# Optimization experiments

Hardware: AMD Instinct MI355X
Metric: run time of the kernel (lower is better)

## Reference

```python
import jax, jax.numpy as jnp
import numpy as np

N, D, C = 8192, 256, 100
MARGIN = 1.0


def setup_inputs() -> dict:
    key = jax.random.key(0)
    k1, k2 = jax.random.split(key)
    features = jax.random.normal(k1, (N, D), dtype=jnp.float32)
    labels = jax.random.randint(k2, (N,), 0, C, dtype=jnp.int64)
    return {"features": features, "labels": labels}


def _pairwise_dist(f):
    # f: [N, D] L2-normalized rows. Euclidean distance matrix [N, N].
    sq = jnp.sum(f * f, axis=1)  # [N]
    d2 = sq[:, None] + sq[None, :] - 2.0 * (f @ f.T)
    d2 = jnp.maximum(d2, 0.0)
    # safe sqrt: zero distance (incl. diagonal) -> 0 with finite grad
    pos = d2 > 0.0
    return jnp.where(pos, jnp.sqrt(jnp.where(pos, d2, 1.0)), 0.0)


def reference(features, labels):
    # F.normalize(p=2, dim=1)
    norm = jnp.linalg.norm(features, axis=1, keepdims=True)
    f = features / jnp.maximum(norm, 1e-12)

    dist = _pairwise_dist(f)  # [N, N]

    onehot = jax.nn.one_hot(labels, C, dtype=f.dtype)  # [N, C]
    counts = jnp.sum(onehot, axis=0)  # [C]
    # S[a, b] = sum_{i in a, j in b} dist[i, j]
    S = onehot.T @ dist @ onehot  # [C, C]

    # intra: per-class mean over off-diagonal pairs (diag of dist is 0),
    # only classes with count > 1, then mean over those classes
    intra_valid = counts > 1.0
    intra_denom = jnp.where(intra_valid, counts * (counts - 1.0), 1.0)
    intra_per_class = jnp.diag(S) / intra_denom
    n_intra = jnp.sum(intra_valid.astype(f.dtype))
    intra = jnp.where(
        n_intra > 0,
        jnp.sum(jnp.where(intra_valid, intra_per_class, 0.0)) / jnp.maximum(n_intra, 1.0),
        0.0,
    )

    # inter: per class-pair (a < b, both present) mean distance, then mean over pairs
    pair_cnt = counts[:, None] * counts[None, :]
    inter_mat = S / jnp.where(pair_cnt > 0.0, pair_cnt, 1.0)
    present = counts > 0.0
    upper = jnp.triu(jnp.ones((C, C), dtype=bool), k=1)
    pair_mask = upper & present[:, None] & present[None, :]
    n_pairs = jnp.sum(pair_mask.astype(f.dtype))
    inter = jnp.where(
        n_pairs > 0,
        jnp.sum(jnp.where(pair_mask, inter_mat, 0.0)) / jnp.maximum(n_pairs, 1.0),
        1.0,
    )

    loss = jax.nn.relu(intra - inter + MARGIN)
    return loss  # scalar; .mean() of a scalar is itself
```

## Files before the change

### kernel.cpp

```cpp
#include <hip/hip_runtime.h>
#include <math.h>

#define N_ROWS 8192
#define D_DIM  256
#define C_CLS  100
#define BM 128
#define NSTRIP (N_ROWS / BM)
#define NBLK (NSTRIP * (NSTRIP + 1) / 2)
#define UPK (C_CLS * (C_CLS + 1) / 2)
#define MAXSEG 4

typedef __attribute__((ext_vector_type(4))) float floatx4;

__device__ __forceinline__ void gl2lds16(const void* g, void* l) {
    __builtin_amdgcn_global_load_lds(
        (const __attribute__((address_space(1))) void*)g,
        (__attribute__((address_space(3))) void*)l, 16, 0, 0);
}

__global__ void sort_k(const int* __restrict__ labels, int* __restrict__ dest,
                       int* __restrict__ slab, int* __restrict__ offs,
                       float* __restrict__ Ug, int* __restrict__ ctr) {
    __shared__ int h[C_CLS];
    __shared__ int incl[128];
    __shared__ int oS[C_CLS + 1];
    __shared__ int cur[C_CLS];
    const int t = threadIdx.x;
    if (t < C_CLS) h[t] = 0;
    __syncthreads();
    int myl[8];
#pragma unroll
    for (int u = 0; u < 8; ++u) myl[u] = labels[t + u * 1024];
#pragma unroll
    for (int u = 0; u < 8; ++u) atomicAdd(&h[myl[u]], 1);
    __syncthreads();
    if (t < 128) {
        const int lane = t & 63;
        int v = (t < C_CLS) ? h[t] : 0;
#pragma unroll
        for (int o = 1; o < 64; o <<= 1) {
            const int n = __shfl_up(v, o, 64);
            if (lane >= o) v += n;
        }
        incl[t] = v;
    }
    __syncthreads();
    if (t <= C_CLS)
        oS[t] = (t == 0) ? 0 : incl[t - 1] + ((t - 1) >= 64 ? incl[63] : 0);
    __syncthreads();
    if (t < C_CLS) cur[t] = oS[t];
    __syncthreads();
#pragma unroll
    for (int u = 0; u < 8; ++u) {
        const int i = t + u * 1024;
        const int pos = atomicAdd(&cur[myl[u]], 1);
        dest[i] = pos;
        slab[pos] = myl[u];
    }
    if (t < C_CLS + 1) offs[t] = oS[t];
    for (int e = t; e < UPK; e += 1024) Ug[e] = 0.f;
    if (t == 0) *ctr = 0;
}

__global__ void normalize_k(const float* __restrict__ in, const int* __restrict__ dest,
                            unsigned int* __restrict__ fnb8) {
    const int row  = blockIdx.x * 4 + (threadIdx.x >> 6);
    const int lane = threadIdx.x & 63;
    float4 v = ((const float4*)in)[row * 64 + lane];
    float s = v.x * v.x + v.y * v.y + v.z * v.z + v.w * v.w;
#pragma unroll
    for (int o = 32; o > 0; o >>= 1) s += __shfl_xor(s, o, 64);
    const float inv = 1.f / fmaxf(sqrtf(s), 1e-12f);
    const int d = dest[row];
    int pk = __builtin_amdgcn_cvt_pk_fp8_f32(v.x * inv, v.y * inv, 0, 0);
    pk     = __builtin_amdgcn_cvt_pk_fp8_f32(v.z * inv, v.w * inv, pk, 1);
    fnb8[d * 64 + lane] = (unsigned int)pk;
}

__global__ __launch_bounds__(256, 2)
void main_k(const unsigned char* __restrict__ fnb8, const int* __restrict__ slab,
            const int* __restrict__ offs_g, float* __restrict__ Ug,
            int* __restrict__ ctr, float* __restrict__ out) {
    __shared__ __align__(16) unsigned char smem[65536];
    unsigned char* const As = smem;
    unsigned char* const Bs = smem + 32768;
    float* const red   = (float*)smem;
    int*   const meta  = (int*)(smem + 4352);
    int*   const flag  = (int*)(smem + 4416);
    float* const rf    = (float*)(smem + 4432);
    int*   const ri    = (int*)(smem + 5456);
    int*   const soffs = (int*)(smem + 6480);

    const int t = threadIdx.x;

    int b = blockIdx.x, ti = 0, len = NSTRIP;
    while (b >= len) { b -= len; ++ti; --len; }
    const int tj = ti + b;
    const int i0 = ti * BM, j0 = tj * BM;

    const int lane = t & 63;
    const int w    = t >> 6;
    const int m0 = (w & 1) * 64, n0 = (w >> 1) * 64;
    const int lr = lane & 15, lq = lane >> 4;
    const int swz = (lr >> 1) & 7;

    int abase[4], bbase[4];
#pragma unroll
    for (int mb = 0; mb < 4; ++mb) abase[mb] = (m0 + mb * 16 + lr) * D_DIM;
#pragma unroll
    for (int nb = 0; nb < 4; ++nb) bbase[nb] = (n0 + nb * 16 + lr) * D_DIM;

#pragma unroll
    for (int u = 0; u < 8; ++u) {
        const int s = t + 256 * u;
        const int row = s >> 4;
        const int kc  = (s & 15) ^ ((row >> 1) & 7);
        gl2lds16(&fnb8[(size_t)(i0 + row) * D_DIM + kc * 16], &As[s * 16]);
    }
#pragma unroll
    for (int u = 0; u < 8; ++u) {
        const int s = t + 256 * u;
        const int row = s >> 4;
        const int kc  = (s & 15) ^ ((row >> 1) & 7);
        gl2lds16(&fnb8[(size_t)(j0 + row) * D_DIM + kc * 16], &Bs[s * 16]);
    }

    floatx4 acc[4][4];
#pragma unroll
    for (int mb = 0; mb < 4; ++mb)
#pragma unroll
        for (int nb = 0; nb < 4; ++nb) acc[mb][nb] = 0.f;

    __syncthreads();

#pragma unroll
    for (int si = 0; si < 8; ++si) {
        const int coff = ((((si * 2) + (lq >> 1)) ^ swz) << 4) + ((lq & 1) << 3);
        long a[4], bb[4];
#pragma unroll
        for (int mb = 0; mb < 4; ++mb) a[mb]  = *(const long*)&As[abase[mb] + coff];
#pragma unroll
        for (int nb = 0; nb < 4; ++nb) bb[nb] = *(const long*)&Bs[bbase[nb] + coff];
#pragma unroll
        for (int mb = 0; mb < 4; ++mb)
#pragma unroll
            for (int nb = 0; nb < 4; ++nb)
                acc[mb][nb] = __builtin_amdgcn_mfma_f32_16x16x32_fp8_fp8(
                    a[mb], bb[nb], acc[mb][nb], 0, 0, 0);
    }

    __syncthreads();

    if (t < C_CLS + 1) soffs[t] = offs_g[t];

    const bool diag = (ti == tj);
#pragma unroll
    for (int mb = 0; mb < 4; ++mb)
#pragma unroll
        for (int nb = 0; nb < 4; ++nb)
#pragma unroll
            for (int r = 0; r < 4; ++r) {
                const float g = acc[mb][nb][r];
                float dv = __builtin_amdgcn_sqrtf(fmaxf(2.f - 2.f * g, 0.f));
                const int rt = m0 + mb * 16 + lq * 4 + r;
                const int ct = n0 + nb * 16 + lr;
                if (diag && rt == ct) dv = 0.f;
                acc[mb][nb][r] = dv;
            }

    const int cA0 = __builtin_amdgcn_readfirstlane(slab[i0 + m0]);
    const int cA1 = __builtin_amdgcn_readfirstlane(slab[i0 + m0 + 63]);
    const int cB0 = __builtin_amdgcn_readfirstlane(slab[j0 + n0]);
    const int cB1 = __builtin_amdgcn_readfirstlane(slab[j0 + n0 + 63]);
    const int segsA = cA1 - cA0 + 1, segsB = cB1 - cB0 + 1;
    if (lane == 0) {
        meta[w * 4 + 0] = cA0; meta[w * 4 + 1] = cB0;
        meta[w * 4 + 2] = segsA; meta[w * 4 + 3] = segsB;
    }
    const float wscale = diag ? 1.f : 2.f;

    float rem[4][4];
#pragma unroll
    for (int mb = 0; mb < 4; ++mb)
#pragma unroll
        for (int r = 0; r < 4; ++r)
            rem[mb][r] = acc[mb][0][r] + acc[mb][1][r] + acc[mb][2][r] + acc[mb][3][r];

    __syncthreads();

    for (int sb = 0; sb < segsB; ++sb) {
        const int cb = cB0 + sb;
        float colsum[4][4];
        if (sb == segsB - 1) {
#pragma unroll
            for (int mb = 0; mb < 4; ++mb)
#pragma unroll
                for (int r = 0; r < 4; ++r) colsum[mb][r] = rem[mb][r];
        } else {
            const int rb0 = max(soffs[cb]     - j0, n0);
            const int rb1 = min(soffs[cb + 1] - j0, n0 + 64);
#pragma unroll
            for (int mb = 0; mb < 4; ++mb)
#pragma unroll
                for (int r = 0; r < 4; ++r) colsum[mb][r] = 0.f;
#pragma unroll
            for (int nb = 0; nb < 4; ++nb) {
                const int ct = n0 + nb * 16 + lr;
                const float mk = ((ct >= rb0) & (ct < rb1)) ? 1.f : 0.f;
#pragma unroll
                for (int mb = 0; mb < 4; ++mb)
#pragma unroll
                    for (int r = 0; r < 4; ++r)
                        colsum[mb][r] = fmaf(mk, acc[mb][nb][r], colsum[mb][r]);
            }
#pragma unroll
            for (int mb = 0; mb < 4; ++mb)
#pragma unroll
                for (int r = 0; r < 4; ++r) rem[mb][r] -= colsum[mb][r];
        }
        for (int sa = 0; sa < segsA; ++sa) {
            const int ca = cA0 + sa;
            const int ra0 = max(soffs[ca]     - i0, m0);
            const int ra1 = min(soffs[ca + 1] - i0, m0 + 64);
            float v = 0.f;
#pragma unroll
            for (int mb = 0; mb < 4; ++mb) {
                const int rtb = m0 + mb * 16 + lq * 4;
#pragma unroll
                for (int r = 0; r < 4; ++r) {
                    const int rt = rtb + r;
                    const bool ir = (rt >= ra0) & (rt < ra1);
                    v += ir ? colsum[mb][r] : 0.f;
                }
            }
            if (sa < MAXSEG && sb < MAXSEG) {
                v += __shfl_xor(v, 1, 64);
                v += __shfl_xor(v, 2, 64);
                if ((lane & 3) == 0)
                    red[(w * 16 + sb * MAXSEG + sa) * 17 + (lane >> 2)] = v;
            } else {
#pragma unroll
                for (int o = 32; o > 0; o >>= 1) v += __shfl_xor(v, o, 64);
                if (lane == 0 && v != 0.f) {
                    const int mn = min(ca, cb), mx = max(ca, cb);
                    atomicAdd(&Ug[mx + ((mn * (2 * C_CLS - 1 - mn)) >> 1)], wscale * v);
                }
            }
        }
    }

    __syncthreads();
    {
        const int combo = t >> 2, q = t & 3;
        const int wv = combo >> 4, sl = combo & 15;
        const float* rp = &red[(wv * 16 + sl) * 17];
        float s = rp[q * 4 + 0] + rp[q * 4 + 1] + rp[q * 4 + 2] + rp[q * 4 + 3];
        s += __shfl_xor(s, 1, 64);
        s += __shfl_xor(s, 2, 64);
        const int sa = sl & (MAXSEG - 1), sb = sl >> 2;
        if (q == 0 && sa < meta[wv * 4 + 2] && sb < meta[wv * 4 + 3] && s != 0.f) {
            const int ca = meta[wv * 4 + 0] + sa, cb = meta[wv * 4 + 1] + sb;
            const int mn = min(ca, cb), mx = max(ca, cb);
            atomicAdd(&Ug[mx + ((mn * (2 * C_CLS - 1 - mn)) >> 1)], wscale * s);
        }
    }

    __syncthreads();
    if (t == 0) {
        asm volatile("s_waitcnt vmcnt(0)" ::: "memory");
        *flag = (atomicAdd(ctr, 1) == NBLK - 1) ? 1 : 0;
    }
    __syncthreads();
    if (*flag) {
        __threadfence();
        float s_intra = 0.f; int n_intra = 0;
        if (t < C_CLS) {
            const int c = soffs[t + 1] - soffs[t];
            if (c > 1) {
                const int idx = t + ((t * (2 * C_CLS - 1 - t)) >> 1);
                s_intra = Ug[idx] / ((float)c * (float)(c - 1));
                n_intra = 1;
            }
        }
        float s_inter = 0.f; int n_pairs = 0;
        for (int p = t; p < C_CLS * C_CLS; p += 256) {
            const int a = p / C_CLS, b2 = p - a * C_CLS;
            if (b2 > a) {
                const int ca = soffs[a + 1] - soffs[a];
                const int cb = soffs[b2 + 1] - soffs[b2];
                if (ca > 0 && cb > 0) {
                    const int idx = b2 + ((a * (2 * C_CLS - 1 - a)) >> 1);
                    s_inter += 0.5f * Ug[idx] / ((float)ca * (float)cb);
                    ++n_pairs;
                }
            }
        }
        rf[t] = s_intra; ri[t] = n_intra; __syncthreads();
        for (int s2 = 128; s2 > 0; s2 >>= 1) {
            if (t < s2) { rf[t] += rf[t + s2]; ri[t] += ri[t + s2]; }
            __syncthreads();
        }
        const float intra_sum = rf[0]; const int intra_n = ri[0];
        __syncthreads();
        rf[t] = s_inter; ri[t] = n_pairs; __syncthreads();
        for (int s2 = 128; s2 > 0; s2 >>= 1) {
            if (t < s2) { rf[t] += rf[t + s2]; ri[t] += ri[t + s2]; }
            __syncthreads();
        }
        if (t == 0) {
            const float inter_sum = rf[0]; const int pairs_n = ri[0];
            const float intra = (intra_n > 0) ? intra_sum / (float)intra_n : 0.f;
            const float inter = (pairs_n > 0) ? inter_sum / (float)pairs_n : 1.f;
            out[0] = fmaxf(intra - inter + 1.0f, 0.f);
        }
    }
}

extern "C" void kernel_launch(void* const* d_in, const int* in_sizes, int n_in,
                              void* d_out, int out_size, void* d_ws, size_t ws_size,
                              hipStream_t stream) {
    const float* feats  = (const float*)d_in[0];
    const int*   labels = (const int*)d_in[1];
    float* out = (float*)d_out;

    char* p = (char*)d_ws;
    unsigned char* fnb8 = (unsigned char*)p;  p += (size_t)N_ROWS * D_DIM;
    int*   slab = (int*)p;  p += (size_t)N_ROWS * sizeof(int);
    int*   dest = (int*)p;  p += (size_t)N_ROWS * sizeof(int);
    int*   offs = (int*)p;  p += 128 * sizeof(int);
    float* Ug   = (float*)p;  p += ((UPK + 31) / 32) * 32 * sizeof(float);
    int*   ctr  = (int*)p;

    sort_k     <<<1, 1024, 0, stream>>>(labels, dest, slab, offs, Ug, ctr);
    normalize_k<<<N_ROWS / 4, 256, 0, stream>>>(feats, dest, (unsigned int*)fnb8);
    main_k     <<<NBLK, 256, 0, stream>>>(fnb8, slab, offs, Ug, ctr, out);
}
```

Before: 124.4 us.

## Fuse sort and normalize into one prep kernel, gather rows via permutation, split K

Merges the label counting-sort and the row normalization into a single launch. Normalized rows are now stored in original order, and the main kernel reads them through a permutation index, so normalization no longer waits on the sort. The main GEMM tile now loads K in two 128-wide chunks, which halves LDS use per block and allows 4 blocks per CU instead of 2. The costs are an indirect row gather, an extra barrier pair per K step, and a one-block sort that runs concurrently with the normalize blocks.

Result: faster. 117.7 us (-5.4%).

```diff
diff --git a/kernel.cpp b/kernel.cpp
--- a/kernel.cpp
+++ b/kernel.cpp
@@ -5,6 +5,7 @@
 #define D_DIM  256
 #define C_CLS  100
 #define BM 128
+#define BK 128
 #define NSTRIP (N_ROWS / BM)
 #define NBLK (NSTRIP * (NSTRIP + 1) / 2)
 #define UPK (C_CLS * (C_CLS + 1) / 2)
@@ -18,78 +19,76 @@
         (__attribute__((address_space(3))) void*)l, 16, 0, 0);
 }
 
-__global__ void sort_k(const int* __restrict__ labels, int* __restrict__ dest,
-                       int* __restrict__ slab, int* __restrict__ offs,
-                       float* __restrict__ Ug, int* __restrict__ ctr) {
-    __shared__ int h[C_CLS];
-    __shared__ int incl[128];
-    __shared__ int oS[C_CLS + 1];
-    __shared__ int cur[C_CLS];
-    const int t = threadIdx.x;
-    if (t < C_CLS) h[t] = 0;
-    __syncthreads();
-    int myl[8];
-#pragma unroll
-    for (int u = 0; u < 8; ++u) myl[u] = labels[t + u * 1024];
-#pragma unroll
-    for (int u = 0; u < 8; ++u) atomicAdd(&h[myl[u]], 1);
-    __syncthreads();
-    if (t < 128) {
-        const int lane = t & 63;
-        int v = (t < C_CLS) ? h[t] : 0;
-#pragma unroll
-        for (int o = 1; o < 64; o <<= 1) {
-            const int n = __shfl_up(v, o, 64);
-            if (lane >= o) v += n;
-        }
-        incl[t] = v;
-    }
-    __syncthreads();
-    if (t <= C_CLS)
-        oS[t] = (t == 0) ? 0 : incl[t - 1] + ((t - 1) >= 64 ? incl[63] : 0);
-    __syncthreads();
-    if (t < C_CLS) cur[t] = oS[t];
-    __syncthreads();
-#pragma unroll
-    for (int u = 0; u < 8; ++u) {
-        const int i = t + u * 1024;
-        const int pos = atomicAdd(&cur[myl[u]], 1);
-        dest[i] = pos;
-        slab[pos] = myl[u];
-    }
-    if (t < C_CLS + 1) offs[t] = oS[t];
-    for (int e = t; e < UPK; e += 1024) Ug[e] = 0.f;
-    if (t == 0) *ctr = 0;
+__global__ __launch_bounds__(256)
+void prep_k(const float* __restrict__ in, const int* __restrict__ labels,
+            unsigned int* __restrict__ fnb8, int* __restrict__ slab,
+            int* __restrict__ offs, int* __restrict__ perm,
+            float* __restrict__ Ug, int* __restrict__ ctr) {
+    if (blockIdx.x == 0) {
+        __shared__ int h[C_CLS];
+        __shared__ int incl[128];
+        __shared__ int oS[C_CLS + 1];
+        __shared__ int cur[C_CLS];
+        const int t = threadIdx.x;
+        if (t < C_CLS) h[t] = 0;
+        __syncthreads();
+        int myl[32];
+#pragma unroll
+        for (int u = 0; u < 32; ++u) myl[u] = labels[t + u * 256];
+#pragma unroll
+        for (int u = 0; u < 32; ++u) atomicAdd(&h[myl[u]], 1);
+        __syncthreads();
+        if (t < 128) {
+            const int lane = t & 63;
+            int v = (t < C_CLS) ? h[t] : 0;
+#pragma unroll
+            for (int o = 1; o < 64; o <<= 1) {
+                const int n = __shfl_up(v, o, 64);
+                if (lane >= o) v += n;
+            }
+            incl[t] = v;
+        }
+        __syncthreads();
+        if (t <= C_CLS)
+            oS[t] = (t == 0) ? 0 : incl[t - 1] + ((t - 1) >= 64 ? incl[63] : 0);
+        __syncthreads();
+        if (t < C_CLS) cur[t] = oS[t];
+        __syncthreads();
+#pragma unroll
+        for (int u = 0; u < 32; ++u) {
+            const int i = t + u * 256;
+            const int pos = atomicAdd(&cur[myl[u]], 1);
+            slab[pos] = myl[u];
+            perm[pos] = i;
+        }
+        if (t < C_CLS + 1) offs[t] = oS[t];
+        for (int e = t; e < UPK; e += 256) Ug[e] = 0.f;
+        if (t == 0) *ctr = 0;
+    } else {
+        const int row  = (blockIdx.x - 1) * 4 + (threadIdx.x >> 6);
+        const int lane = threadIdx.x & 63;
+        float4 v = ((const float4*)in)[row * 64 + lane];
+        float s = v.x * v.x + v.y * v.y + v.z * v.z + v.w * v.w;
+#pragma unroll
+        for (int o = 32; o > 0; o >>= 1) s += __shfl_xor(s, o, 64);
+        const float inv = 1.f / fmaxf(sqrtf(s), 1e-12f);
+        int pk = __builtin_amdgcn_cvt_pk_fp8_f32(v.x * inv, v.y * inv, 0, 0);
+        pk     = __builtin_amdgcn_cvt_pk_fp8_f32(v.z * inv, v.w * inv, pk, 1);
+        fnb8[row * 64 + lane] = (unsigned int)pk;
+    }
 }
 
-__global__ void normalize_k(const float* __restrict__ in, const int* __restrict__ dest,
-                            unsigned int* __restrict__ fnb8) {
-    const int row  = blockIdx.x * 4 + (threadIdx.x >> 6);
-    const int lane = threadIdx.x & 63;
-    float4 v = ((const float4*)in)[row * 64 + lane];
-    float s = v.x * v.x + v.y * v.y + v.z * v.z + v.w * v.w;
-#pragma unroll
-    for (int o = 32; o > 0; o >>= 1) s += __shfl_xor(s, o, 64);
-    const float inv = 1.f / fmaxf(sqrtf(s), 1e-12f);
-    const int d = dest[row];
-    int pk = __builtin_amdgcn_cvt_pk_fp8_f32(v.x * inv, v.y * inv, 0, 0);
-    pk     = __builtin_amdgcn_cvt_pk_fp8_f32(v.z * inv, v.w * inv, pk, 1);
-    fnb8[d * 64 + lane] = (unsigned int)pk;
-}
-
-__global__ __launch_bounds__(256, 2)
+__global__ __launch_bounds__(256, 4)
 void main_k(const unsigned char* __restrict__ fnb8, const int* __restrict__ slab,
-            const int* __restrict__ offs_g, float* __restrict__ Ug,
-            int* __restrict__ ctr, float* __restrict__ out) {
-    __shared__ __align__(16) unsigned char smem[65536];
-    unsigned char* const As = smem;
-    unsigned char* const Bs = smem + 32768;
-    float* const red   = (float*)smem;
-    int*   const meta  = (int*)(smem + 4352);
-    int*   const flag  = (int*)(smem + 4416);
-    float* const rf    = (float*)(smem + 4432);
-    int*   const ri    = (int*)(smem + 5456);
-    int*   const soffs = (int*)(smem + 6480);
+            const int* __restrict__ offs_g, const int* __restrict__ perm,
+            float* __restrict__ Ug, int* __restrict__ ctr,
+            float* __restrict__ out) {
+    __shared__ __align__(16) unsigned char As[BM * BK];
+    __shared__ __align__(16) unsigned char Bs[BM * BK];
+    __shared__ float red[4][MAXSEG * MAXSEG][17];
+    __shared__ int soffs[C_CLS + 1];
+    __shared__ int meta[4][4];
+    __shared__ int flagS;
 
     const int t = threadIdx.x;
 
@@ -97,6 +96,8 @@
     while (b >= len) { b -= len; ++ti; --len; }
     const int tj = ti + b;
     const int i0 = ti * BM, j0 = tj * BM;
+
+    if (t < C_CLS + 1) soffs[t] = offs_g[t];
 
     const int lane = t & 63;
     const int w    = t >> 6;
@@ -106,24 +107,21 @@
 
     int abase[4], bbase[4];
 #pragma unroll
-    for (int mb = 0; mb < 4; ++mb) abase[mb] = (m0 + mb * 16 + lr) * D_DIM;
-#pragma unroll
-    for (int nb = 0; nb < 4; ++nb) bbase[nb] = (n0 + nb * 16 + lr) * D_DIM;
-
-#pragma unroll
-    for (int u = 0; u < 8; ++u) {
+    for (int mb = 0; mb < 4; ++mb) abase[mb] = (m0 + mb * 16 + lr) * BK;
+#pragma unroll
+    for (int nb = 0; nb < 4; ++nb) bbase[nb] = (n0 + nb * 16 + lr) * BK;
+
+    int srow[4], skc[4], pA[4], pB[4];
+#pragma unroll
+    for (int u = 0; u < 4; ++u) {
         const int s = t + 256 * u;
-        const int row = s >> 4;
-        const int kc  = (s & 15) ^ ((row >> 1) & 7);
-        gl2lds16(&fnb8[(size_t)(i0 + row) * D_DIM + kc * 16], &As[s * 16]);
-    }
-#pragma unroll
-    for (int u = 0; u < 8; ++u) {
-        const int s = t + 256 * u;
-        const int row = s >> 4;
-        const int kc  = (s & 15) ^ ((row >> 1) & 7);
-        gl2lds16(&fnb8[(size_t)(j0 + row) * D_DIM + kc * 16], &Bs[s * 16]);
-    }
+        srow[u] = s >> 3;
+        skc[u]  = (s & 7) ^ ((srow[u] >> 1) & 7);
+    }
+#pragma unroll
+    for (int u = 0; u < 4; ++u) pA[u] = perm[i0 + srow[u]];
+#pragma unroll
+    for (int u = 0; u < 4; ++u) pB[u] = perm[j0 + srow[u]];
 
     floatx4 acc[4][4];
 #pragma unroll
@@ -131,27 +129,35 @@
 #pragma unroll
         for (int nb = 0; nb < 4; ++nb) acc[mb][nb] = 0.f;
 
-    __syncthreads();
-
-#pragma unroll
-    for (int si = 0; si < 8; ++si) {
-        const int coff = ((((si * 2) + (lq >> 1)) ^ swz) << 4) + ((lq & 1) << 3);
-        long a[4], bb[4];
-#pragma unroll
-        for (int mb = 0; mb < 4; ++mb) a[mb]  = *(const long*)&As[abase[mb] + coff];
-#pragma unroll
-        for (int nb = 0; nb < 4; ++nb) bb[nb] = *(const long*)&Bs[bbase[nb] + coff];
-#pragma unroll
-        for (int mb = 0; mb < 4; ++mb)
-#pragma unroll
-            for (int nb = 0; nb < 4; ++nb)
-                acc[mb][nb] = __builtin_amdgcn_mfma_f32_16x16x32_fp8_fp8(
-                    a[mb], bb[nb], acc[mb][nb], 0, 0, 0);
-    }
-
-    __syncthreads();
-
-    if (t < C_CLS + 1) soffs[t] = offs_g[t];
+#pragma unroll
+    for (int k0 = 0; k0 < D_DIM; k0 += BK) {
+        __syncthreads();
+#pragma unroll
+        for (int u = 0; u < 4; ++u)
+            gl2lds16(&fnb8[((size_t)pA[u] << 8) + k0 + skc[u] * 16],
+                     &As[(t + 256 * u) * 16]);
+#pragma unroll
+        for (int u = 0; u < 4; ++u)
+            gl2lds16(&fnb8[((size_t)pB[u] << 8) + k0 + skc[u] * 16],
+                     &Bs[(t + 256 * u) * 16]);
+        __syncthreads();
+
+#pragma unroll
+        for (int si = 0; si < 4; ++si) {
+            const int coff = ((((si * 2) + (lq >> 1)) ^ swz) << 4) + ((lq & 1) << 3);
+            long a[4], bb[4];
+#pragma unroll
+            for (int mb = 0; mb < 4; ++mb) a[mb]  = *(const long*)&As[abase[mb] + coff];
+#pragma unroll
+            for (int nb = 0; nb < 4; ++nb) bb[nb] = *(const long*)&Bs[bbase[nb] + coff];
+#pragma unroll
+            for (int mb = 0; mb < 4; ++mb)
+#pragma unroll
+                for (int nb = 0; nb < 4; ++nb)
+                    acc[mb][nb] = __builtin_amdgcn_mfma_f32_16x16x32_fp8_fp8(
+                        a[mb], bb[nb], acc[mb][nb], 0, 0, 0);
+        }
+    }
 
     const bool diag = (ti == tj);
 #pragma unroll
@@ -174,8 +180,7 @@
     const int cB1 = __builtin_amdgcn_readfirstlane(slab[j0 + n0 + 63]);
     const int segsA = cA1 - cA0 + 1, segsB = cB1 - cB0 + 1;
     if (lane == 0) {
-        meta[w * 4 + 0] = cA0; meta[w * 4 + 1] = cB0;
-        meta[w * 4 + 2] = segsA; meta[w * 4 + 3] = segsB;
+        meta[w][0] = cA0; meta[w][1] = cB0; meta[w][2] = segsA; meta[w][3] = segsB;
     }
     const float wscale = diag ? 1.f : 2.f;
 
@@ -185,8 +190,6 @@
 #pragma unroll
         for (int r = 0; r < 4; ++r)
             rem[mb][r] = acc[mb][0][r] + acc[mb][1][r] + acc[mb][2][r] + acc[mb][3][r];
-
-    __syncthreads();
 
     for (int sb = 0; sb < segsB; ++sb) {
         const int cb = cB0 + sb;
@@ -236,8 +239,7 @@
             if (sa < MAXSEG && sb < MAXSEG) {
                 v += __shfl_xor(v, 1, 64);
                 v += __shfl_xor(v, 2, 64);
-                if ((lane & 3) == 0)
-                    red[(w * 16 + sb * MAXSEG + sa) * 17 + (lane >> 2)] = v;
+                if ((lane & 3) == 0) red[w][sb * MAXSEG + sa][lane >> 2] = v;
             } else {
 #pragma unroll
                 for (int o = 32; o > 0; o >>= 1) v += __shfl_xor(v, o, 64);
@@ -253,13 +255,13 @@
     {
         const int combo = t >> 2, q = t & 3;
         const int wv = combo >> 4, sl = combo & 15;
-        const float* rp = &red[(wv * 16 + sl) * 17];
-        float s = rp[q * 4 + 0] + rp[q * 4 + 1] + rp[q * 4 + 2] + rp[q * 4 + 3];
+        float s = red[wv][sl][q * 4 + 0] + red[wv][sl][q * 4 + 1]
+                + red[wv][sl][q * 4 + 2] + red[wv][sl][q * 4 + 3];
         s += __shfl_xor(s, 1, 64);
         s += __shfl_xor(s, 2, 64);
         const int sa = sl & (MAXSEG - 1), sb = sl >> 2;
-        if (q == 0 && sa < meta[wv * 4 + 2] && sb < meta[wv * 4 + 3] && s != 0.f) {
-            const int ca = meta[wv * 4 + 0] + sa, cb = meta[wv * 4 + 1] + sb;
+        if (q == 0 && sa < meta[wv][2] && sb < meta[wv][3] && s != 0.f) {
+            const int ca = meta[wv][0] + sa, cb = meta[wv][1] + sb;
             const int mn = min(ca, cb), mx = max(ca, cb);
             atomicAdd(&Ug[mx + ((mn * (2 * C_CLS - 1 - mn)) >> 1)], wscale * s);
         }
@@ -268,10 +270,12 @@
     __syncthreads();
     if (t == 0) {
         asm volatile("s_waitcnt vmcnt(0)" ::: "memory");
-        *flag = (atomicAdd(ctr, 1) == NBLK - 1) ? 1 : 0;
+        flagS = (atomicAdd(ctr, 1) == NBLK - 1) ? 1 : 0;
     }
     __syncthreads();
-    if (*flag) {
+    if (flagS) {
+        float* const rf = (float*)&red[0][0][0];
+        int*   const ri = (int*)&red[2][0][0];
         __threadfence();
         float s_intra = 0.f; int n_intra = 0;
         if (t < C_CLS) {
@@ -326,12 +330,12 @@
     char* p = (char*)d_ws;
     unsigned char* fnb8 = (unsigned char*)p;  p += (size_t)N_ROWS * D_DIM;
     int*   slab = (int*)p;  p += (size_t)N_ROWS * sizeof(int);
-    int*   dest = (int*)p;  p += (size_t)N_ROWS * sizeof(int);
+    int*   perm = (int*)p;  p += (size_t)N_ROWS * sizeof(int);
     int*   offs = (int*)p;  p += 128 * sizeof(int);
     float* Ug   = (float*)p;  p += ((UPK + 31) / 32) * 32 * sizeof(float);
     int*   ctr  = (int*)p;
 
-    sort_k     <<<1, 1024, 0, stream>>>(labels, dest, slab, offs, Ug, ctr);
-    normalize_k<<<N_ROWS / 4, 256, 0, stream>>>(feats, dest, (unsigned int*)fnb8);
-    main_k     <<<NBLK, 256, 0, stream>>>(fnb8, slab, offs, Ug, ctr, out);
+    prep_k <<<1 + N_ROWS / 4, 256, 0, stream>>>(feats, labels, (unsigned int*)fnb8,
+                                                slab, offs, perm, Ug, ctr);
+    main_k <<<NBLK, 256, 0, stream>>>(fnb8, slab, offs, perm, Ug, ctr, out);
 }
```
